# Kernel tuning notes

Hardware: AMD Instinct MI355X
Metric: run time of the kernel (lower is better)

Reference implementation:

```python
import jax, jax.numpy as jnp
import numpy as np

B, C, L, D, E, K = 64, 23, 26000, 64, 512, 3  # batch, chromosomes, bins/chr, d_model, eos_dim, num_states
V = C * L


def setup_inputs() -> dict:
    key = jax.random.key(0)
    k0, k1, k2, k3 = jax.random.split(key, 4)
    return {
        "eos_emb": jax.random.normal(k0, (B, C, E), jnp.float32),
        "bin_ids": jnp.arange(C * L, dtype=jnp.int32).reshape(C, L),
        "emb_table": jax.random.normal(k1, (V, D), jnp.float32) * 0.02,
        "eos_W": jax.random.normal(k2, (D, E), jnp.float32) / np.float32(np.sqrt(E)),
        "eos_b": jnp.zeros((D,), jnp.float32),
        "fc_W": jax.random.normal(k3, (K, 2 * D), jnp.float32) / np.float32(np.sqrt(2 * D)),
        "fc_b": jnp.zeros((K,), jnp.float32),
    }


def reference(eos_emb, bin_ids, emb_table, eos_W, eos_b, fc_W, fc_b):
    # eos_projection (use_eos_proj=True): [B,C,E] @ [D,E]^T + b -> [B,C,D]
    eos = jnp.einsum('bce,de->bcd', eos_emb, eos_W) + eos_b
    # per-chromosome embedding gather (bin_projection skipped: bin_emb_dim == d_model, use_bin_proj=False)
    bin_emb = emb_table[bin_ids]  # [C,L,D]
    # fc on concat([bin, eos]) == bin @ Wb^T + eos @ We^T + b (avoids materializing [B,C,L,2D])
    Wb, We = fc_W[:, :D], fc_W[:, D:]
    a = jnp.einsum('cld,kd->clk', bin_emb, Wb)          # [C,L,K]
    e = jnp.einsum('bcd,kd->bck', eos, We) + fc_b       # [B,C,K]
    return jax.nn.relu(a[None, :, :, :] + e[:, :, None, :])  # [B,C,L,K]
```

## Files before the change

### kernel.cpp

```cpp
#include <hip/hip_runtime.h>

#define NB 64
#define NC 23
#define NL 26000
#define ND 64
#define NE 512
#define NK 3
#define FP4   (NL * NK / 4)
#define CFP4  (NC * FP4)
#define CHUNK 3504
#define NCHUNK 128
#define NJ 14

typedef float v4f __attribute__((ext_vector_type(4)));

__global__ __launch_bounds__(256) void eos_e_kernel(
    const float* __restrict__ eos_emb,
    const float* __restrict__ eos_W,
    const float* __restrict__ eos_b,
    const float* __restrict__ fc_W,
    const float* __restrict__ fc_b,
    float* __restrict__ e_out)
{
    const int bc = blockIdx.x;
    const int t  = threadIdx.x;
    const int q  = t & 3;
    const int d  = t >> 2;

    __shared__ v4f xs4[NE / 4];
    if (t < NE / 4)
        xs4[t] = reinterpret_cast<const v4f*>(eos_emb + (size_t)bc * NE)[t];
    __syncthreads();

    const v4f* wrow = reinterpret_cast<const v4f*>(eos_W + (size_t)d * NE);
    v4f acc = (v4f)(0.f);
    #pragma unroll 8
    for (int j = 0; j < NE / 16; ++j) {
        const int idx = q + 4 * j;
        acc += wrow[idx] * xs4[idx];
    }
    float p = (acc.x + acc.y) + (acc.z + acc.w);
    p += __shfl_xor(p, 1, 64);
    p += __shfl_xor(p, 2, 64);
    const float eosd = p + eos_b[d];

    __shared__ float part[4][NK];
    #pragma unroll
    for (int k = 0; k < NK; ++k) {
        float pk = eosd * fc_W[k * (2 * ND) + ND + d];
        pk += __shfl_xor(pk,  4, 64);
        pk += __shfl_xor(pk,  8, 64);
        pk += __shfl_xor(pk, 16, 64);
        pk += __shfl_xor(pk, 32, 64);
        if ((t & 63) == 0) part[t >> 6][k] = pk;
    }
    __syncthreads();
    if (t < NK)
        e_out[(size_t)bc * NK + t] =
            part[0][t] + part[1][t] + part[2][t] + part[3][t] + fc_b[t];
}

__global__ __launch_bounds__(256) void a_kernel(
    const int*   __restrict__ bin_ids,
    const float* __restrict__ emb_table,
    const float* __restrict__ fc_W,
    float* __restrict__ a_out)
{
    const int c = blockIdx.y;
    const int t = threadIdx.x;
    const int q = t & 3;
    const int r = t >> 2;
    const int l = blockIdx.x * 64 + r;

    __shared__ v4f wb4[NK][ND / 4];
    if (t < NK * (ND / 4)) {
        const int k = t / (ND / 4), i = t % (ND / 4);
        wb4[k][i] = reinterpret_cast<const v4f*>(fc_W + (size_t)k * (2 * ND))[i];
    }
    __syncthreads();
    if (l >= NL) return;

    const int row = bin_ids[(size_t)c * NL + l];
    const v4f* er = reinterpret_cast<const v4f*>(emb_table + (size_t)row * ND);

    v4f s0 = (v4f)(0.f), s1 = (v4f)(0.f), s2 = (v4f)(0.f);
    #pragma unroll
    for (int j = 0; j < 4; ++j) {
        const int idx = q + 4 * j;
        const v4f v = er[idx];
        s0 += v * wb4[0][idx];
        s1 += v * wb4[1][idx];
        s2 += v * wb4[2][idx];
    }
    float a0 = (s0.x + s0.y) + (s0.z + s0.w);
    float a1 = (s1.x + s1.y) + (s1.z + s1.w);
    float a2 = (s2.x + s2.y) + (s2.z + s2.w);
    a0 += __shfl_xor(a0, 1, 64); a0 += __shfl_xor(a0, 2, 64);
    a1 += __shfl_xor(a1, 1, 64); a1 += __shfl_xor(a1, 2, 64);
    a2 += __shfl_xor(a2, 1, 64); a2 += __shfl_xor(a2, 2, 64);

    if (q < NK) {
        const float val = (q == 0) ? a0 : (q == 1) ? a1 : a2;
        a_out[((size_t)c * NL + l) * NK + q] = val;
    }
}

__global__ __launch_bounds__(256) void bcopy_kernel(
    const float* __restrict__ a_in,
    const float* __restrict__ e_in,
    float* __restrict__ out)
{
    const int b    = blockIdx.x;
    const int cx   = blockIdx.y;
    const int t    = threadIdx.x;
    const int base = cx * CHUNK;

    const int c_lo = base / FP4;
    const int c_hi_raw = (base + CHUNK - 1) / FP4;
    const int c_hi = (c_hi_raw < NC) ? c_hi_raw : (NC - 1);
    const int c_split = (c_lo + 1) * FP4;

    __shared__ v4f e4[3][2];
    if (t < 6) {
        const int p = t >> 1, ci = t & 1;
        const int c = ci ? c_hi : c_lo;
        const float* ep = e_in + ((size_t)b * NC + c) * NK;
        const float e0 = ep[0], e1 = ep[1], e2 = ep[2];
        v4f v;
        if      (p == 0) { v.x = e0; v.y = e1; v.z = e2; v.w = e0; }
        else if (p == 1) { v.x = e1; v.y = e2; v.z = e0; v.w = e1; }
        else             { v.x = e2; v.y = e0; v.z = e1; v.w = e2; }
        e4[p][ci] = v;
    }
    __syncthreads();

    const v4f* a4 = reinterpret_cast<const v4f*>(a_in);
    v4f* o4 = reinterpret_cast<v4f*>(out) + (size_t)b * CFP4;

    #pragma unroll
    for (int j = 0; j < NJ; ++j) {
        const int fo = j * 256 + t;
        const int f  = base + fo;
        if (fo < CHUNK && f < CFP4) {
            const v4f av = a4[f];
            const v4f ev = e4[f % 3][(f >= c_split) ? 1 : 0];
            v4f o;
            o.x = fmaxf(av.x + ev.x, 0.f);
            o.y = fmaxf(av.y + ev.y, 0.f);
            o.z = fmaxf(av.z + ev.z, 0.f);
            o.w = fmaxf(av.w + ev.w, 0.f);
            o4[f] = o;
        }
    }
}

__global__ __launch_bounds__(256) void decoder_fused_kernel(
    const int*   __restrict__ bin_ids,
    const float* __restrict__ emb_table,
    const float* __restrict__ fc_W,
    const float* __restrict__ e_in,
    float* __restrict__ out)
{
    const int c   = blockIdx.y;
    const int tid = threadIdx.x;
    const int l   = blockIdx.x * 256 + tid;

    __shared__ float wb[NK][ND];
    __shared__ float es[NB * NK];

    if (tid < NK * ND)
        wb[tid / ND][tid % ND] = fc_W[(tid / ND) * (2 * ND) + (tid % ND)];
    if (tid < NB * NK) {
        int b = tid / NK, k = tid % NK;
        es[tid] = e_in[((size_t)b * NC + c) * NK + k];
    }
    __syncthreads();
    if (l >= NL) return;

    const int row = bin_ids[(size_t)c * NL + l];
    const float4* er = reinterpret_cast<const float4*>(emb_table + (size_t)row * ND);
    const float4* w0 = reinterpret_cast<const float4*>(wb[0]);
    const float4* w1 = reinterpret_cast<const float4*>(wb[1]);
    const float4* w2 = reinterpret_cast<const float4*>(wb[2]);

    float a0 = 0.f, a1 = 0.f, a2 = 0.f;
    #pragma unroll
    for (int i = 0; i < ND / 4; ++i) {
        float4 v  = er[i];
        float4 p0 = w0[i], p1 = w1[i], p2 = w2[i];
        a0 += v.x * p0.x + v.y * p0.y + v.z * p0.z + v.w * p0.w;
        a1 += v.x * p1.x + v.y * p1.y + v.z * p1.z + v.w * p1.w;
        a2 += v.x * p2.x + v.y * p2.y + v.z * p2.z + v.w * p2.w;
    }

    size_t obase = ((size_t)c * NL + l) * NK;
    const size_t bstride = (size_t)NC * NL * NK;
    #pragma unroll 4
    for (int b = 0; b < NB; ++b) {
        const float e0 = es[b * NK + 0];
        const float e1 = es[b * NK + 1];
        const float e2 = es[b * NK + 2];
        out[obase + 0] = fmaxf(a0 + e0, 0.f);
        out[obase + 1] = fmaxf(a1 + e1, 0.f);
        out[obase + 2] = fmaxf(a2 + e2, 0.f);
        obase += bstride;
    }
}

extern "C" void kernel_launch(void* const* d_in, const int* in_sizes, int n_in,
                              void* d_out, int out_size, void* d_ws, size_t ws_size,
                              hipStream_t stream) {
    const float* eos_emb   = (const float*)d_in[0];
    const int*   bin_ids   = (const int*)  d_in[1];
    const float* emb_table = (const float*)d_in[2];
    const float* eos_W     = (const float*)d_in[3];
    const float* eos_b     = (const float*)d_in[4];
    const float* fc_W      = (const float*)d_in[5];
    const float* fc_b      = (const float*)d_in[6];
    float*       out       = (float*)d_out;

    float*  e_ws = (float*)d_ws;
    const size_t a_off_bytes = 32768;
    float*  a_ws = (float*)((char*)d_ws + a_off_bytes);
    const size_t a_bytes = (size_t)NC * NL * NK * sizeof(float);

    eos_e_kernel<<<NB * NC, 256, 0, stream>>>(eos_emb, eos_W, eos_b, fc_W, fc_b, e_ws);

    if (ws_size >= a_off_bytes + a_bytes) {
        dim3 grid_a((NL + 63) / 64, NC);
        a_kernel<<<grid_a, 256, 0, stream>>>(bin_ids, emb_table, fc_W, a_ws);

        dim3 grid_b(NB, NCHUNK);
        bcopy_kernel<<<grid_b, 256, 0, stream>>>(a_ws, e_ws, out);
    } else {
        dim3 grid((NL + 255) / 256, NC);
        decoder_fused_kernel<<<grid, 256, 0, stream>>>(bin_ids, emb_table, fc_W, e_ws, out);
    }
}
```

Measured before the change: 167.2 us.

## Fuse bin projection and batch broadcast into a single kernel via LDS

Replaces the separate a_kernel and bcopy_kernel with one kernel that computes the per-bin projection for a chunk of flattened outputs into shared memory, then writes the relu-broadcast result for all batches. This removes the round trip of the intermediate a array through global memory and one kernel launch. In exchange each block recomputes a few boundary rows, uses smaller blocks, and each thread loops over all batches serially.

```diff
diff --git a/kernel.cpp b/kernel.cpp
--- a/kernel.cpp
+++ b/kernel.cpp
@@ -8,9 +8,9 @@
 #define NK 3
 #define FP4   (NL * NK / 4)
 #define CFP4  (NC * FP4)
-#define CHUNK 3504
-#define NCHUNK 128
-#define NJ 14
+#define CH    128
+#define NBLKF ((CFP4 + CH - 1) / CH)
+#define NBC   (NB * NC)
 
 typedef float v4f __attribute__((ext_vector_type(4)));
 
@@ -60,96 +60,98 @@
             part[0][t] + part[1][t] + part[2][t] + part[3][t] + fc_b[t];
 }
 
-__global__ __launch_bounds__(256) void a_kernel(
+__global__ __launch_bounds__(128) void fused2_kernel(
     const int*   __restrict__ bin_ids,
     const float* __restrict__ emb_table,
     const float* __restrict__ fc_W,
-    float* __restrict__ a_out)
+    const float* __restrict__ e_in,
+    float* __restrict__ out)
 {
-    const int c = blockIdx.y;
-    const int t = threadIdx.x;
-    const int q = t & 3;
-    const int r = t >> 2;
-    const int l = blockIdx.x * 64 + r;
-
-    __shared__ v4f wb4[NK][ND / 4];
+    const int bx = blockIdx.x;
+    const int t  = threadIdx.x;
+    const int base   = bx * CH;
+    const int nvalid = (CFP4 - base < CH) ? (CFP4 - base) : CH;
+    const int nfl    = nvalid * 4;
+
+    __shared__ v4f   wb4[NK][ND / 4];
+    __shared__ float a_lds[CH * 4];
+    __shared__ v4f   e4[3][2][65];
+
     if (t < NK * (ND / 4)) {
         const int k = t / (ND / 4), i = t % (ND / 4);
         wb4[k][i] = reinterpret_cast<const v4f*>(fc_W + (size_t)k * (2 * ND))[i];
     }
-    __syncthreads();
-    if (l >= NL) return;
-
-    const int row = bin_ids[(size_t)c * NL + l];
-    const v4f* er = reinterpret_cast<const v4f*>(emb_table + (size_t)row * ND);
-
-    v4f s0 = (v4f)(0.f), s1 = (v4f)(0.f), s2 = (v4f)(0.f);
-    #pragma unroll
-    for (int j = 0; j < 4; ++j) {
-        const int idx = q + 4 * j;
-        const v4f v = er[idx];
-        s0 += v * wb4[0][idx];
-        s1 += v * wb4[1][idx];
-        s2 += v * wb4[2][idx];
-    }
-    float a0 = (s0.x + s0.y) + (s0.z + s0.w);
-    float a1 = (s1.x + s1.y) + (s1.z + s1.w);
-    float a2 = (s2.x + s2.y) + (s2.z + s2.w);
-    a0 += __shfl_xor(a0, 1, 64); a0 += __shfl_xor(a0, 2, 64);
-    a1 += __shfl_xor(a1, 1, 64); a1 += __shfl_xor(a1, 2, 64);
-    a2 += __shfl_xor(a2, 1, 64); a2 += __shfl_xor(a2, 2, 64);
-
-    if (q < NK) {
-        const float val = (q == 0) ? a0 : (q == 1) ? a1 : a2;
-        a_out[((size_t)c * NL + l) * NK + q] = val;
-    }
-}
-
-__global__ __launch_bounds__(256) void bcopy_kernel(
-    const float* __restrict__ a_in,
-    const float* __restrict__ e_in,
-    float* __restrict__ out)
-{
-    const int b    = blockIdx.x;
-    const int cx   = blockIdx.y;
-    const int t    = threadIdx.x;
-    const int base = cx * CHUNK;
-
     const int c_lo = base / FP4;
-    const int c_hi_raw = (base + CHUNK - 1) / FP4;
-    const int c_hi = (c_hi_raw < NC) ? c_hi_raw : (NC - 1);
-    const int c_split = (c_lo + 1) * FP4;
-
-    __shared__ v4f e4[3][2];
-    if (t < 6) {
-        const int p = t >> 1, ci = t & 1;
-        const int c = ci ? c_hi : c_lo;
-        const float* ep = e_in + ((size_t)b * NC + c) * NK;
+    const int c_hi = (base + nvalid - 1) / FP4;
+    for (int it = t; it < 3 * 2 * NB; it += 128) {
+        const int p   = it / (2 * NB);
+        const int rem = it - p * (2 * NB);
+        const int ci  = rem >> 6;
+        const int bl  = rem & 63;
+        const int c   = ci ? c_hi : c_lo;
+        const float* ep = e_in + ((size_t)bl * NC + c) * NK;
         const float e0 = ep[0], e1 = ep[1], e2 = ep[2];
         v4f v;
         if      (p == 0) { v.x = e0; v.y = e1; v.z = e2; v.w = e0; }
         else if (p == 1) { v.x = e1; v.y = e2; v.z = e0; v.w = e1; }
         else             { v.x = e2; v.y = e0; v.z = e1; v.w = e2; }
-        e4[p][ci] = v;
-    }
-    __syncthreads();
-
-    const v4f* a4 = reinterpret_cast<const v4f*>(a_in);
-    v4f* o4 = reinterpret_cast<v4f*>(out) + (size_t)b * CFP4;
-
+        e4[p][ci][bl] = v;
+    }
+    __syncthreads();
+
+    const int q = t & 3;
+    const int r = t >> 2;
+    const int gl_lo  = (4 * base) / 3;
+    const int gl_end = (4 * base + nfl + 2) / 3;
+    const int nrows  = gl_end - gl_lo;
     #pragma unroll
-    for (int j = 0; j < NJ; ++j) {
-        const int fo = j * 256 + t;
-        const int f  = base + fo;
-        if (fo < CHUNK && f < CFP4) {
-            const v4f av = a4[f];
-            const v4f ev = e4[f % 3][(f >= c_split) ? 1 : 0];
+    for (int pass = 0; pass < 6; ++pass) {
+        const int rl = pass * 32 + r;
+        if (rl < nrows) {
+            const int gl  = gl_lo + rl;
+            const int row = bin_ids[gl];
+            const v4f* er = reinterpret_cast<const v4f*>(emb_table + (size_t)row * ND);
+            v4f s0 = (v4f)(0.f), s1 = (v4f)(0.f), s2 = (v4f)(0.f);
+            #pragma unroll
+            for (int j = 0; j < 4; ++j) {
+                const int idx = q + 4 * j;
+                const v4f v = er[idx];
+                s0 += v * wb4[0][idx];
+                s1 += v * wb4[1][idx];
+                s2 += v * wb4[2][idx];
+            }
+            float a0 = (s0.x + s0.y) + (s0.z + s0.w);
+            float a1 = (s1.x + s1.y) + (s1.z + s1.w);
+            float a2 = (s2.x + s2.y) + (s2.z + s2.w);
+            a0 += __shfl_xor(a0, 1, 64); a0 += __shfl_xor(a0, 2, 64);
+            a1 += __shfl_xor(a1, 1, 64); a1 += __shfl_xor(a1, 2, 64);
+            a2 += __shfl_xor(a2, 1, 64); a2 += __shfl_xor(a2, 2, 64);
+            if (q < NK) {
+                const float val = (q == 0) ? a0 : (q == 1) ? a1 : a2;
+                const int j = 3 * gl + q - 4 * base;
+                if (j >= 0 && j < nfl) a_lds[j] = val;
+            }
+        }
+    }
+    __syncthreads();
+
+    if (t < nvalid) {
+        const int f = base + t;
+        const v4f av = *reinterpret_cast<const v4f*>(&a_lds[t * 4]);
+        const int p  = f % 3;
+        const int ci = ((f / FP4) > c_lo) ? 1 : 0;
+        const v4f* eptr = &e4[p][ci][0];
+        v4f* o4 = reinterpret_cast<v4f*>(out) + f;
+        #pragma unroll 4
+        for (int bl = 0; bl < NB; ++bl) {
+            const v4f ev = eptr[bl];
             v4f o;
             o.x = fmaxf(av.x + ev.x, 0.f);
             o.y = fmaxf(av.y + ev.y, 0.f);
             o.z = fmaxf(av.z + ev.z, 0.f);
             o.w = fmaxf(av.w + ev.w, 0.f);
-            o4[f] = o;
+            *o4 = o;
+            o4 += CFP4;
         }
     }
 }
@@ -219,19 +221,12 @@
     const float* fc_b      = (const float*)d_in[6];
     float*       out       = (float*)d_out;
 
-    float*  e_ws = (float*)d_ws;
-    const size_t a_off_bytes = 32768;
-    float*  a_ws = (float*)((char*)d_ws + a_off_bytes);
-    const size_t a_bytes = (size_t)NC * NL * NK * sizeof(float);
-
-    eos_e_kernel<<<NB * NC, 256, 0, stream>>>(eos_emb, eos_W, eos_b, fc_W, fc_b, e_ws);
-
-    if (ws_size >= a_off_bytes + a_bytes) {
-        dim3 grid_a((NL + 63) / 64, NC);
-        a_kernel<<<grid_a, 256, 0, stream>>>(bin_ids, emb_table, fc_W, a_ws);
-
-        dim3 grid_b(NB, NCHUNK);
-        bcopy_kernel<<<grid_b, 256, 0, stream>>>(a_ws, e_ws, out);
+    float* e_ws = (float*)d_ws;
+
+    eos_e_kernel<<<NBC, 256, 0, stream>>>(eos_emb, eos_W, eos_b, fc_W, fc_b, e_ws);
+
+    if (ws_size >= (size_t)NBC * NK * sizeof(float)) {
+        fused2_kernel<<<NBLKF, 128, 0, stream>>>(bin_ids, emb_table, fc_W, e_ws, out);
     } else {
         dim3 grid((NL + 255) / 256, NC);
         decoder_fused_kernel<<<grid, 256, 0, stream>>>(bin_ids, emb_table, fc_W, e_ws, out);
```

New measurement: 161.1 us. 3.6% less time.
